# Kernel tuning notes

Hardware: AMD Instinct MI355X
Metric: run time of the kernel (lower is better)

The kernel has to match this reference:

```python
import jax, jax.numpy as jnp
import numpy as np


def setup_inputs() -> dict:
    key = jax.random.key(0)
    k_x, k_m, k_w1, k_b1, k_w2, k_b2 = jax.random.split(key, 6)
    b, seq_len, d_in, d_out = 8, 4096, 1024, 512
    x = jax.random.normal(k_x, (b, seq_len, d_in), dtype=jnp.float32)
    # binary-ish mask in {0,1} as floats (torch code multiplies by mask)
    mask = (jax.random.uniform(k_m, (b, seq_len)) < 0.5).astype(jnp.float32)
    s1 = 1.0 / np.sqrt(d_in)
    s2 = 1.0 / np.sqrt(d_out)
    W_enc = jax.random.uniform(k_w1, (d_out, d_in), minval=-s1, maxval=s1, dtype=jnp.float32)
    b_enc = jax.random.uniform(k_b1, (d_out,), minval=-s1, maxval=s1, dtype=jnp.float32)
    W_dec = jax.random.uniform(k_w2, (d_in, d_out), minval=-s2, maxval=s2, dtype=jnp.float32)
    b_dec = jax.random.uniform(k_b2, (d_in,), minval=-s2, maxval=s2, dtype=jnp.float32)
    return {"x": x, "mask": mask, "W_enc": W_enc, "b_enc": b_enc, "W_dec": W_dec, "b_dec": b_dec}


def reference(x, mask, W_enc, b_enc, W_dec, b_dec):
    # per-step: v_t = v_{t-1} + relu(x_t @ W_enc^T + b_enc) * mask_t  -> additive scan == cumsum
    h = jax.nn.relu(jnp.einsum('bsd,od->bso', x, W_enc) + b_enc) * mask[:, :, None]  # [b,s,d_out]
    v_cum = jnp.cumsum(h, axis=1)  # [b,s,d_out]
    out_enc = jnp.einsum('bso,do->bsd', v_cum, W_dec) + b_dec  # decode every prefix state
    v = v_cum[:, -1, :]  # final accumulated state
    return (v, out_enc)
```

## Files before the change

kernel.cpp:

```cpp
#include <hip/hip_runtime.h>
#include <hip/hip_bf16.h>
#include <stdint.h>

typedef __bf16 bf16_t;
typedef __bf16 bf16x4 __attribute__((ext_vector_type(4)));
typedef __bf16 bf16x8 __attribute__((ext_vector_type(8)));
typedef float  f32x4  __attribute__((ext_vector_type(4)));

__device__ __forceinline__ void gload_lds16(const void* g, void* l) {
  __builtin_amdgcn_global_load_lds(
      (__attribute__((address_space(1))) void*)g,
      (__attribute__((address_space(3))) void*)l, 16, 0, 0);
}

__global__ void cast_weights(const float* __restrict__ a, bf16_t* __restrict__ oa,
                             const float* __restrict__ b, bf16_t* __restrict__ ob,
                             int n4each) {
  const int i = blockIdx.x * blockDim.x + threadIdx.x;
  const float* src; bf16_t* dst; int k;
  if (i < n4each) { src = a; dst = oa; k = i; }
  else            { src = b; dst = ob; k = i - n4each; }
  f32x4 v = reinterpret_cast<const f32x4*>(src)[k];
  bf16x4 o;
  o[0] = (bf16_t)v[0]; o[1] = (bf16_t)v[1]; o[2] = (bf16_t)v[2]; o[3] = (bf16_t)v[3];
  reinterpret_cast<bf16x4*>(dst)[k] = o;
}

#define PHASE_SYNC() do { \
  __builtin_amdgcn_s_barrier(); \
  asm volatile("s_waitcnt lgkmcnt(0)" ::: "memory"); \
  __builtin_amdgcn_sched_barrier(0); \
  __builtin_amdgcn_s_setprio(1); \
} while (0)

#define PHASE_END() do { \
  __builtin_amdgcn_s_setprio(0); \
  __builtin_amdgcn_s_barrier(); \
} while (0)

#define QUAD(RH, CH, BF) do { \
  _Pragma("unroll") \
  for (int fr = 0; fr < 4; ++fr) { \
    _Pragma("unroll") \
    for (int fc = 0; fc < 2; ++fc) { \
      acc[RH][CH][fr][fc] = __builtin_amdgcn_mfma_f32_16x16x32_bf16(a[fr][0], BF[fc][0], acc[RH][CH][fr][fc], 0, 0, 0); \
      acc[RH][CH][fr][fc] = __builtin_amdgcn_mfma_f32_16x16x32_bf16(a[fr][1], BF[fc][1], acc[RH][CH][fr][fc], 0, 0, 0); \
    } \
  } \
} while (0)

__global__ __launch_bounds__(512, 2) void gemm1_f8p(
    const float* __restrict__ x, const bf16_t* __restrict__ Wenc,
    const float* __restrict__ b_enc, const float* __restrict__ mask,
    bf16_t* __restrict__ h_out, float* __restrict__ partials)
{
  __shared__ __align__(16) char smem[131072];
  float* Af = (float*)smem;
  auto Bl = [&](int buf) { return (bf16_t*)(smem + 65536 + buf * 32768); };

  const int tid  = threadIdx.x;
  const int lane = tid & 63;
  const int w    = tid >> 6;
  const int wm   = w >> 2;
  const int wn   = w & 3;
  const long bm  = (long)blockIdx.x * 256;
  const long bn  = (long)blockIdx.y * 256;
  const int NT   = 16;

  f32x4  acc[2][2][4][2] = {};
  bf16x8 a[4][2], b0[2][2], b1[2][2];

  const int scolB = (((lane & 7) ^ (lane >> 3)) << 3);
  auto stageB = [&](int t, int h) {
    bf16_t* lb = Bl(t & 1);
    #pragma unroll
    for (int c = 0; c < 2; ++c) {
      const int r0 = h * 128 + (w * 2 + c) * 8;
      gload_lds16(Wenc + (bn + r0 + (lane >> 3)) * 1024 + t * 64 + scolB, lb + r0 * 64);
    }
  };
  auto stageA = [&](int t, int h) {
    #pragma unroll
    for (int c = 0; c < 4; ++c) {
      const int r0  = h * 128 + w * 16 + c * 4;
      const int row = r0 + (lane >> 4);
      const int sblk = (lane & 15) ^ (row & 15);
      gload_lds16(x + (bm + row) * 1024 + t * 64 + sblk * 4, Af + r0 * 64);
    }
  };
  auto loadAf = [&](int rh) {
    #pragma unroll
    for (int fr = 0; fr < 4; ++fr) {
      const int row = rh * 128 + wm * 64 + fr * 16 + (lane & 15);
      const float* rp = Af + row * 64;
      #pragma unroll
      for (int kx = 0; kx < 2; ++kx) {
        const int g0 = kx * 8 + (lane >> 4) * 2;
        f32x4 lo = *reinterpret_cast<const f32x4*>(rp + (((g0    ) ^ (lane & 15)) << 2));
        f32x4 hi = *reinterpret_cast<const f32x4*>(rp + (((g0 + 1) ^ (lane & 15)) << 2));
        bf16x8 o;
        #pragma unroll
        for (int e = 0; e < 4; ++e) { o[e] = (bf16_t)lo[e]; o[e + 4] = (bf16_t)hi[e]; }
        a[fr][kx] = o;
      }
    }
  };
  const int fcb0 = ((((lane >> 4)    ) ^ (lane & 7)) << 3);
  const int fcb1 = ((((lane >> 4) + 4) ^ (lane & 7)) << 3);
  auto loadB = [&](int buf, int ch, bf16x8 (&bf)[2][2]) {
    const bf16_t* lb = Bl(buf);
    #pragma unroll
    for (int fc = 0; fc < 2; ++fc) {
      const int row = ch * 128 + wn * 32 + fc * 16 + (lane & 15);
      bf[fc][0] = *reinterpret_cast<const bf16x8*>(lb + row * 64 + fcb0);
      bf[fc][1] = *reinterpret_cast<const bf16x8*>(lb + row * 64 + fcb1);
    }
  };

  __builtin_amdgcn_sched_barrier(0);
  stageA(0, 0); stageA(0, 1); stageB(0, 0); stageB(0, 1);
  stageB(1, 0); stageB(1, 1);
  asm volatile("s_waitcnt vmcnt(4)" ::: "memory");
  __builtin_amdgcn_s_barrier();

  for (int t = 0; t < NT; ++t) {
    const int buf = t & 1;
    const bool g1 = (t + 1 < NT);
    const bool g2 = (t + 2 < NT);

    loadAf(0); loadB(buf, 0, b0);
    PHASE_SYNC(); QUAD(0, 0, b0); PHASE_END();

    loadB(buf, 1, b1);
    if (g1) stageA(t + 1, 0);
    if (g2) stageB(t + 2, 0);
    PHASE_SYNC(); QUAD(0, 1, b1);
    __builtin_amdgcn_s_setprio(0);
    if (g2)      asm volatile("s_waitcnt vmcnt(6)" ::: "memory");
    else if (g1) asm volatile("s_waitcnt vmcnt(4)" ::: "memory");
    else         asm volatile("s_waitcnt vmcnt(0)" ::: "memory");
    __builtin_amdgcn_s_barrier();

    loadAf(1);
    if (g2) stageB(t + 2, 1);
    PHASE_SYNC(); QUAD(1, 0, b0); PHASE_END();

    if (g1) stageA(t + 1, 1);
    PHASE_SYNC(); QUAD(1, 1, b1);
    __builtin_amdgcn_s_setprio(0);
    if (g2)      asm volatile("s_waitcnt vmcnt(8)" ::: "memory");
    else if (g1) asm volatile("s_waitcnt vmcnt(4)" ::: "memory");
    else         asm volatile("s_waitcnt vmcnt(0)" ::: "memory");
    __builtin_amdgcn_s_barrier();
  }
  asm volatile("s_waitcnt vmcnt(0) lgkmcnt(0)" ::: "memory");
  __builtin_amdgcn_s_barrier();
  __builtin_amdgcn_sched_barrier(0);

  bf16_t* tile = (bf16_t*)smem;
  float bv[2][2];
  #pragma unroll
  for (int ch = 0; ch < 2; ++ch)
    #pragma unroll
    for (int fc = 0; fc < 2; ++fc)
      bv[ch][fc] = b_enc[bn + ch * 128 + wn * 32 + fc * 16 + (lane & 15)];

  #pragma unroll
  for (int rh = 0; rh < 2; ++rh)
    #pragma unroll
    for (int fr = 0; fr < 4; ++fr) {
      const int row0 = rh * 128 + wm * 64 + fr * 16 + ((lane >> 4) << 2);
      const f32x4 mv = *reinterpret_cast<const f32x4*>(&mask[bm + row0]);
      #pragma unroll
      for (int ch = 0; ch < 2; ++ch)
        #pragma unroll
        for (int fc = 0; fc < 2; ++fc) {
          const int col = ch * 128 + wn * 32 + fc * 16 + (lane & 15);
          #pragma unroll
          for (int e = 0; e < 4; ++e) {
            const int row = row0 + e;
            float hv = acc[rh][ch][fr][fc][e] + bv[ch][fc];
            hv = (hv > 0.f ? hv : 0.f) * mv[e];
            tile[row * 256 + (col ^ (((row >> 2) & 3) << 4))] = (bf16_t)hv;
          }
        }
    }
  __syncthreads();

  const int sub = tid >> 8;
  const int col = tid & 255;
  float run = 0.f;
  bf16_t* hp = h_out + (bm + sub * 128) * 512 + bn + col;
  #pragma unroll 4
  for (int s = 0; s < 128; ++s) {
    const int row = sub * 128 + s;
    run += (float)tile[row * 256 + (col ^ (((row >> 2) & 3) << 4))];
    hp[(long)s * 512] = (bf16_t)run;
  }
  partials[(blockIdx.x * 2 + sub) * 512 + bn + col] = run;
}

__global__ __launch_bounds__(512, 2) void gemm2_8p(
    const bf16_t* __restrict__ A, const bf16_t* __restrict__ B,
    const int K, const int N,
    const float* __restrict__ Padd,
    float* __restrict__ outf)
{
  __shared__ __align__(16) char smem[131072];

  const int tid  = threadIdx.x;
  const int lane = tid & 63;
  const int w    = tid >> 6;
  const int wm   = w >> 2;
  const int wn   = w & 3;
  const long bm  = (long)blockIdx.x * 256;
  const long bn  = (long)blockIdx.y * 256;
  const int NT   = K >> 6;

  const int scol = (((lane & 7) ^ (lane >> 3)) << 3);
  const int fcb0 = ((((lane >> 4)    ) ^ (lane & 7)) << 3);
  const int fcb1 = ((((lane >> 4) + 4) ^ (lane & 7)) << 3);

  f32x4  acc[2][2][4][2] = {};
  bf16x8 a[4][2], b0[2][2], b1[2][2];

  auto Albs = [&](int buf) { return (bf16_t*)(smem + buf * 65536); };
  auto Blbs = [&](int buf) { return (bf16_t*)(smem + buf * 65536 + 32768); };

  auto stageA = [&](int t, int h) {
    bf16_t* lb = Albs(t & 1);
    #pragma unroll
    for (int c = 0; c < 2; ++c) {
      const int r0 = h * 128 + (w * 2 + c) * 8;
      gload_lds16(A + (bm + r0 + (lane >> 3)) * (long)K + t * 64 + scol, lb + r0 * 64);
    }
  };
  auto stageB = [&](int t, int h) {
    bf16_t* lb = Blbs(t & 1);
    #pragma unroll
    for (int c = 0; c < 2; ++c) {
      const int r0 = h * 128 + (w * 2 + c) * 8;
      gload_lds16(B + (bn + r0 + (lane >> 3)) * (long)K + t * 64 + scol, lb + r0 * 64);
    }
  };
  auto loadA = [&](int buf, int rh) {
    const bf16_t* lb = Albs(buf);
    #pragma unroll
    for (int fr = 0; fr < 4; ++fr) {
      const int row = rh * 128 + wm * 64 + fr * 16 + (lane & 15);
      a[fr][0] = *reinterpret_cast<const bf16x8*>(lb + row * 64 + fcb0);
      a[fr][1] = *reinterpret_cast<const bf16x8*>(lb + row * 64 + fcb1);
    }
  };
  auto loadB = [&](int buf, int ch, bf16x8 (&bf)[2][2]) {
    const bf16_t* lb = Blbs(buf);
    #pragma unroll
    for (int fc = 0; fc < 2; ++fc) {
      const int row = ch * 128 + wn * 32 + fc * 16 + (lane & 15);
      bf[fc][0] = *reinterpret_cast<const bf16x8*>(lb + row * 64 + fcb0);
      bf[fc][1] = *reinterpret_cast<const bf16x8*>(lb + row * 64 + fcb1);
    }
  };

  __builtin_amdgcn_sched_barrier(0);
  stageA(0, 0); stageA(0, 1); stageB(0, 0); stageB(0, 1);
  stageA(1, 0); stageA(1, 1); stageB(1, 0); stageB(1, 1);
  asm volatile("s_waitcnt vmcnt(8)" ::: "memory");
  __builtin_amdgcn_s_barrier();

  for (int t = 0; t < NT; ++t) {
    const int buf = t & 1;
    const bool g2 = (t + 2 < NT);

    loadA(buf, 0); loadB(buf, 0, b0);
    PHASE_SYNC(); QUAD(0, 0, b0); PHASE_END();

    loadB(buf, 1, b1);
    if (g2) stageA(t + 2, 0);
    PHASE_SYNC(); QUAD(0, 1, b1); PHASE_END();

    loadA(buf, 1);
    if (g2) stageB(t + 2, 0);
    PHASE_SYNC(); QUAD(1, 0, b0); PHASE_END();

    if (g2) { stageA(t + 2, 1); stageB(t + 2, 1); }
    PHASE_SYNC(); QUAD(1, 1, b1);
    __builtin_amdgcn_s_setprio(0);
    if (g2) asm volatile("s_waitcnt vmcnt(8)" ::: "memory");
    else    asm volatile("s_waitcnt vmcnt(0)" ::: "memory");
    __builtin_amdgcn_s_barrier();
  }
  __builtin_amdgcn_sched_barrier(0);

  #pragma unroll
  for (int rh = 0; rh < 2; ++rh)
    #pragma unroll
    for (int ch = 0; ch < 2; ++ch)
      #pragma unroll
      for (int fc = 0; fc < 2; ++fc) {
        const long gc = bn + ch * 128 + wn * 32 + fc * 16 + (lane & 15);
        const float pv = Padd[(blockIdx.x * 2 + rh) * (long)N + gc];
        #pragma unroll
        for (int fr = 0; fr < 4; ++fr) {
          const long gr = bm + rh * 128 + wm * 64 + fr * 16 + ((lane >> 4) << 2);
          #pragma unroll
          for (int e = 0; e < 4; ++e)
            outf[(gr + e) * (long)N + gc] = acc[rh][ch][fr][fc][e] + pv;
        }
      }
}

__global__ __launch_bounds__(256) void gemm_p(
    const bf16_t* __restrict__ A, const bf16_t* __restrict__ B,
    const int K, const int N,
    const float* __restrict__ bias,
    float* __restrict__ outf)
{
  __shared__ __align__(16) bf16_t As[2][128 * 64];
  __shared__ __align__(16) bf16_t Bs[2][128 * 64];

  const int tid  = threadIdx.x;
  const int lane = tid & 63;
  const int w    = tid >> 6;
  const int wm   = w >> 1, wn = w & 1;
  const long bm  = (long)blockIdx.x * 128;
  const long bn  = (long)blockIdx.y * 128;

  f32x4 acc[4][4] = {};

  const int srow = w * 32 + (lane >> 3);
  const int scol = (lane & 7) * 8;
  const bf16_t* Abase = A + (bm + srow) * (long)K + scol;
  const bf16_t* Bbase = B + (bn + srow) * (long)K + scol;

  auto stage = [&](bf16_t* da, bf16_t* db, int kt) {
    #pragma unroll
    for (int it = 0; it < 4; ++it) {
      gload_lds16(Abase + (long)it * 8 * K + kt, &da[(w * 32 + it * 8) * 64]);
      gload_lds16(Bbase + (long)it * 8 * K + kt, &db[(w * 32 + it * 8) * 64]);
    }
  };
  auto mfma_tile = [&](const bf16_t* Asb, const bf16_t* Bsb) {
    #pragma unroll
    for (int kk = 0; kk < 2; ++kk) {
      const int kof = kk * 32 + (lane >> 4) * 8;
      bf16x8 afr[4], bfr[4];
      #pragma unroll
      for (int i = 0; i < 4; ++i)
        afr[i] = *reinterpret_cast<const bf16x8*>(&Asb[(wm * 64 + i * 16 + (lane & 15)) * 64 + kof]);
      #pragma unroll
      for (int j = 0; j < 4; ++j)
        bfr[j] = *reinterpret_cast<const bf16x8*>(&Bsb[(wn * 64 + j * 16 + (lane & 15)) * 64 + kof]);
      #pragma unroll
      for (int i = 0; i < 4; ++i)
        #pragma unroll
        for (int j = 0; j < 4; ++j)
          acc[i][j] = __builtin_amdgcn_mfma_f32_16x16x32_bf16(afr[i], bfr[j], acc[i][j], 0, 0, 0);
    }
  };

  stage(As[0], Bs[0], 0);
  __syncthreads();
  int kt = 64;
  for (int p2 = 0; p2 < (K >> 7); ++p2) {
    if (kt < K) stage(As[1], Bs[1], kt);
    mfma_tile(As[0], Bs[0]);
    __syncthreads();
    kt += 64;
    if (kt < K) stage(As[0], Bs[0], kt);
    mfma_tile(As[1], Bs[1]);
    __syncthreads();
    kt += 64;
  }

  #pragma unroll
  for (int j = 0; j < 4; ++j) {
    const long gc = bn + wn * 64 + j * 16 + (lane & 15);
    const float addv = bias[gc];
    #pragma unroll
    for (int i = 0; i < 4; ++i) {
      const long gr0 = bm + wm * 64 + i * 16 + ((lane >> 4) << 2);
      #pragma unroll
      for (int r = 0; r < 4; ++r)
        outf[(gr0 + r) * (long)N + gc] = acc[i][j][r] + addv;
    }
  }
}

__global__ void scan_chunks(const float* __restrict__ partials, bf16_t* __restrict__ prefixb,
                            float* __restrict__ v_out) {
  const int idx = blockIdx.x * blockDim.x + threadIdx.x;
  const int b = idx >> 9;
  const int o = idx & 511;
  float run = 0.f;
  #pragma unroll
  for (int c = 0; c < 32; ++c) {
    const size_t off = ((size_t)(b * 32 + c)) * 512 + o;
    prefixb[off] = (bf16_t)run;
    run += partials[off];
  }
  v_out[idx] = run;
}

extern "C" void kernel_launch(void* const* d_in, const int* in_sizes, int n_in,
                              void* d_out, int out_size, void* d_ws, size_t ws_size,
                              hipStream_t stream) {
  const float* x     = (const float*)d_in[0];
  const float* mask  = (const float*)d_in[1];
  const float* W_enc = (const float*)d_in[2];
  const float* b_enc = (const float*)d_in[3];
  const float* W_dec = (const float*)d_in[4];
  const float* b_dec = (const float*)d_in[5];

  float* out     = (float*)d_out;
  float* v_out   = out;
  float* out_enc = out + 4096;

  char* ws = (char*)d_ws;
  bf16_t* Web      = (bf16_t*)ws;  ws += (size_t)512 * 1024 * 2;
  bf16_t* Wdb      = (bf16_t*)ws;  ws += (size_t)1024 * 512 * 2;
  bf16_t* h        = (bf16_t*)ws;  ws += (size_t)32768 * 512 * 2;
  float*  partials = (float*)ws;   ws += (size_t)256 * 512 * 4;
  bf16_t* prefixb  = (bf16_t*)ws;  ws += (size_t)256 * 512 * 2;
  float*  P        = (float*)ws;   ws += (size_t)256 * 1024 * 4;

  cast_weights<<<1024, 256, 0, stream>>>(W_enc, Web, W_dec, Wdb, 131072);

  gemm1_f8p<<<dim3(128, 2), 512, 0, stream>>>(x, Web, b_enc, mask, h, partials);

  scan_chunks<<<16, 256, 0, stream>>>(partials, prefixb, v_out);

  gemm_p<<<dim3(2, 8), 256, 0, stream>>>(prefixb, Wdb, 512, 1024, b_dec, P);

  gemm2_8p<<<dim3(128, 4), 512, 0, stream>>>(h, Wdb, 512, 1024, P, out_enc);
}
```

Baseline: 138.9 us.

## Stage x through registers, converting to bf16 once before the LDS write

```diff
diff --git a/kernel.cpp b/kernel.cpp
--- a/kernel.cpp
+++ b/kernel.cpp
@@ -55,7 +55,7 @@
     bf16_t* __restrict__ h_out, float* __restrict__ partials)
 {
   __shared__ __align__(16) char smem[131072];
-  float* Af = (float*)smem;
+  auto Al = [&](int buf) { return (bf16_t*)(smem + buf * 32768); };
   auto Bl = [&](int buf) { return (bf16_t*)(smem + 65536 + buf * 32768); };
 
   const int tid  = threadIdx.x;
@@ -69,6 +69,7 @@
 
   f32x4  acc[2][2][4][2] = {};
   bf16x8 a[4][2], b0[2][2], b1[2][2];
+  f32x4  av[8];
 
   const int scolB = (((lane & 7) ^ (lane >> 3)) << 3);
   auto stageB = [&](int t, int h) {
@@ -79,34 +80,37 @@
       gload_lds16(Wenc + (bn + r0 + (lane >> 3)) * 1024 + t * 64 + scolB, lb + r0 * 64);
     }
   };
-  auto stageA = [&](int t, int h) {
-    #pragma unroll
-    for (int c = 0; c < 4; ++c) {
-      const int r0  = h * 128 + w * 16 + c * 4;
-      const int row = r0 + (lane >> 4);
-      const int sblk = (lane & 15) ^ (row & 15);
-      gload_lds16(x + (bm + row) * 1024 + t * 64 + sblk * 4, Af + r0 * 64);
-    }
-  };
-  auto loadAf = [&](int rh) {
+  auto gaLoad = [&](int t) {
+    #pragma unroll
+    for (int u = 0; u < 8; ++u) {
+      const int row = u * 32 + (tid >> 4);
+      av[u] = *reinterpret_cast<const f32x4*>(x + (bm + row) * 1024 + t * 64 + (tid & 15) * 4);
+    }
+  };
+  auto aWrite = [&](int t) {
+    bf16_t* lb = Al(t & 1);
+    const int c4 = tid & 15;
+    #pragma unroll
+    for (int u = 0; u < 8; ++u) {
+      const int row = u * 32 + (tid >> 4);
+      bf16x4 o;
+      o[0] = (bf16_t)av[u][0]; o[1] = (bf16_t)av[u][1];
+      o[2] = (bf16_t)av[u][2]; o[3] = (bf16_t)av[u][3];
+      *reinterpret_cast<bf16x4*>(lb + row * 64 + ((((c4 >> 1) ^ (row & 7)) << 3) + (c4 & 1) * 4)) = o;
+    }
+  };
+
+  const int fcb0 = ((((lane >> 4)    ) ^ (lane & 7)) << 3);
+  const int fcb1 = ((((lane >> 4) + 4) ^ (lane & 7)) << 3);
+  auto loadA = [&](int buf, int rh) {
+    const bf16_t* lb = Al(buf);
     #pragma unroll
     for (int fr = 0; fr < 4; ++fr) {
       const int row = rh * 128 + wm * 64 + fr * 16 + (lane & 15);
-      const float* rp = Af + row * 64;
-      #pragma unroll
-      for (int kx = 0; kx < 2; ++kx) {
-        const int g0 = kx * 8 + (lane >> 4) * 2;
-        f32x4 lo = *reinterpret_cast<const f32x4*>(rp + (((g0    ) ^ (lane & 15)) << 2));
-        f32x4 hi = *reinterpret_cast<const f32x4*>(rp + (((g0 + 1) ^ (lane & 15)) << 2));
-        bf16x8 o;
-        #pragma unroll
-        for (int e = 0; e < 4; ++e) { o[e] = (bf16_t)lo[e]; o[e + 4] = (bf16_t)hi[e]; }
-        a[fr][kx] = o;
-      }
-    }
-  };
-  const int fcb0 = ((((lane >> 4)    ) ^ (lane & 7)) << 3);
-  const int fcb1 = ((((lane >> 4) + 4) ^ (lane & 7)) << 3);
+      a[fr][0] = *reinterpret_cast<const bf16x8*>(lb + row * 64 + fcb0);
+      a[fr][1] = *reinterpret_cast<const bf16x8*>(lb + row * 64 + fcb1);
+    }
+  };
   auto loadB = [&](int buf, int ch, bf16x8 (&bf)[2][2]) {
     const bf16_t* lb = Bl(buf);
     #pragma unroll
@@ -118,9 +122,11 @@
   };
 
   __builtin_amdgcn_sched_barrier(0);
-  stageA(0, 0); stageA(0, 1); stageB(0, 0); stageB(0, 1);
+  stageB(0, 0); stageB(0, 1);
+  gaLoad(0);
   stageB(1, 0); stageB(1, 1);
-  asm volatile("s_waitcnt vmcnt(4)" ::: "memory");
+  aWrite(0);
+  asm volatile("s_waitcnt lgkmcnt(0)" ::: "memory");
   __builtin_amdgcn_s_barrier();
 
   for (int t = 0; t < NT; ++t) {
@@ -128,29 +134,22 @@
     const bool g1 = (t + 1 < NT);
     const bool g2 = (t + 2 < NT);
 
-    loadAf(0); loadB(buf, 0, b0);
+    if (g1) gaLoad(t + 1);
+    loadA(buf, 0); loadB(buf, 0, b0);
     PHASE_SYNC(); QUAD(0, 0, b0); PHASE_END();
 
     loadB(buf, 1, b1);
-    if (g1) stageA(t + 1, 0);
     if (g2) stageB(t + 2, 0);
-    PHASE_SYNC(); QUAD(0, 1, b1);
-    __builtin_amdgcn_s_setprio(0);
-    if (g2)      asm volatile("s_waitcnt vmcnt(6)" ::: "memory");
-    else if (g1) asm volatile("s_waitcnt vmcnt(4)" ::: "memory");
-    else         asm volatile("s_waitcnt vmcnt(0)" ::: "memory");
-    __builtin_amdgcn_s_barrier();
-
-    loadAf(1);
+    PHASE_SYNC(); QUAD(0, 1, b1); PHASE_END();
+
+    loadA(buf, 1);
     if (g2) stageB(t + 2, 1);
     PHASE_SYNC(); QUAD(1, 0, b0); PHASE_END();
 
-    if (g1) stageA(t + 1, 1);
+    if (g1) aWrite(t + 1);
     PHASE_SYNC(); QUAD(1, 1, b1);
     __builtin_amdgcn_s_setprio(0);
-    if (g2)      asm volatile("s_waitcnt vmcnt(8)" ::: "memory");
-    else if (g1) asm volatile("s_waitcnt vmcnt(4)" ::: "memory");
-    else         asm volatile("s_waitcnt vmcnt(0)" ::: "memory");
+    asm volatile("s_waitcnt vmcnt(4)" ::: "memory");
     __builtin_amdgcn_s_barrier();
   }
   asm volatile("s_waitcnt vmcnt(0) lgkmcnt(0)" ::: "memory");
```

Result: slower. 142.7 us (+2.7%).
